# Kernel optimization log

Measured on AMD Instinct MI355X. Metric: run time of the kernel, lower is better.

## Reference

```python
import jax, jax.numpy as jnp
import numpy as np

DT = 0.1    # arg.DELTA_T
BOX = 1.0   # arg.WORLD_SIZE
B = 8388608


def range_angle(ang):
    # wrap angle to [-pi, pi)
    return jnp.mod(ang + np.pi, 2.0 * np.pi) - np.pi


def setup_inputs() -> dict:
    key = jax.random.key(0)
    k1, k2, k3, k4, k5, k6 = jax.random.split(key, 6)
    x = jax.random.normal(k1, (B, 5), dtype=jnp.float32)          # [px,py,ang,vel,ang_vel]
    a = jax.random.uniform(k2, (B, 2), dtype=jnp.float32)          # actions [a_v, a_w]
    noise = jax.random.normal(k3, (B, 2), dtype=jnp.float32)       # standard-normal process noise
    pro_gains = jax.random.uniform(k4, (2,), dtype=jnp.float32)    # process gains
    pro_noise_ln_vars = jax.random.normal(k5, (2,), dtype=jnp.float32)  # log-variances
    goal_radius = jax.random.uniform(k6, (1,), dtype=jnp.float32)
    return {"x": x, "a": a, "noise": noise, "pro_gains": pro_gains,
            "pro_noise_ln_vars": pro_noise_ln_vars, "goal_radius": goal_radius}


def reference(x, a, noise, pro_gains, pro_noise_ln_vars, goal_radius):
    px, py, ang = x[:, 0], x[:, 1], x[:, 2]
    # w = sqrt(exp(ln_var)) * randn(2)  (noise pre-sampled, deterministic)
    std = jnp.sqrt(jnp.exp(pro_noise_ln_vars))            # [2]
    w = std * noise                                        # [B,2]
    vel = pro_gains[0] * a[:, 0] + w[:, 0]                 # 0*vel drops old vel
    ang_vel = pro_gains[1] * a[:, 1] + w[:, 1]
    ang = range_angle(ang + ang_vel * DT)
    px = jnp.clip(px + vel * jnp.cos(ang) * DT, -BOX, BOX)
    py = jnp.clip(py + vel * jnp.sin(ang) * DT, -BOX, BOX)
    next_x = jnp.stack([px, py, ang, vel, ang_vel], axis=-1)   # [B,5]
    reached_target = jnp.sqrt(px * px + py * py) <= goal_radius[0]  # [B] bool
    return next_x, reached_target
```

## Files before the change

### kernel.cpp

```cpp
#include <hip/hip_runtime.h>
#include <math.h>


__global__ __launch_bounds__(256) void step_kernel(
    const float* __restrict__ x,
    const float* __restrict__ a,
    const float* __restrict__ noise,
    const float* __restrict__ pro_gains,
    const float* __restrict__ pro_noise_ln_vars,
    const float* __restrict__ goal_radius,
    float* __restrict__ out_next,
    float* __restrict__ out_reach,
    int n)
{
    int i = blockIdx.x * blockDim.x + threadIdx.x;
    if (i >= n) return;

    const float g0 = pro_gains[0];
    const float g1 = pro_gains[1];
    const float std0 = __fsqrt_rn(expf(pro_noise_ln_vars[0]));
    const float std1 = __fsqrt_rn(expf(pro_noise_ln_vars[1]));
    const float gr = goal_radius[0];

    const size_t si = (size_t)i;
    const float2 av = *(const float2*)(a + 2 * si);
    const float2 nv = *(const float2*)(noise + 2 * si);
    const float px0  = x[5 * si + 0];
    const float py0  = x[5 * si + 1];
    const float ang0 = x[5 * si + 2];

    const float w0 = __fmul_rn(std0, nv.x);
    const float w1 = __fmul_rn(std1, nv.y);
    const float vel     = __fadd_rn(__fmul_rn(g0, av.x), w0);
    const float ang_vel = __fadd_rn(__fmul_rn(g1, av.y), w1);

    const float DT     = 0.1f;
    const float PI_F   = 3.14159265358979323846f;
    const float TWOPI  = 6.283185307179586f;

    const float t  = __fadd_rn(ang0, __fmul_rn(ang_vel, DT));
    const float tp = __fadd_rn(t, PI_F);
    float m = fmodf(tp, TWOPI);
    if (m < 0.0f) m = __fadd_rn(m, TWOPI);
    const float ang = __fsub_rn(m, PI_F);

    float s, c;
    sincosf(ang, &s, &c);

    float px = __fadd_rn(px0, __fmul_rn(__fmul_rn(vel, c), DT));
    px = fminf(fmaxf(px, -1.0f), 1.0f);
    float py = __fadd_rn(py0, __fmul_rn(__fmul_rn(vel, s), DT));
    py = fminf(fmaxf(py, -1.0f), 1.0f);

    const float r2 = __fadd_rn(__fmul_rn(px, px), __fmul_rn(py, py));
    const float r  = __fsqrt_rn(r2);

    out_next[5 * si + 0] = px;
    out_next[5 * si + 1] = py;
    out_next[5 * si + 2] = ang;
    out_next[5 * si + 3] = vel;
    out_next[5 * si + 4] = ang_vel;
    out_reach[si] = (r <= gr) ? 1.0f : 0.0f;
}

extern "C" void kernel_launch(void* const* d_in, const int* in_sizes, int n_in,
                              void* d_out, int out_size, void* d_ws, size_t ws_size,
                              hipStream_t stream) {
    const float* x      = (const float*)d_in[0];
    const float* a      = (const float*)d_in[1];
    const float* noise  = (const float*)d_in[2];
    const float* gains  = (const float*)d_in[3];
    const float* lnvars = (const float*)d_in[4];
    const float* gradius= (const float*)d_in[5];

    const int n = in_sizes[0] / 5;
    float* out_next  = (float*)d_out;
    float* out_reach = (float*)d_out + (size_t)n * 5;

    const int block = 256;
    const int grid = (n + block - 1) / block;
    step_kernel<<<grid, block, 0, stream>>>(x, a, noise, gains, lnvars, gradius,
                                            out_next, out_reach, n);
}
```

Baseline: 395.3 us.

## Use grid-stride loop with software prefetch of next element's inputs

```diff
diff --git a/kernel.cpp b/kernel.cpp
--- a/kernel.cpp
+++ b/kernel.cpp
@@ -13,72 +13,98 @@
     float* __restrict__ out_reach,
     int n)
 {
+    const int stride = gridDim.x * blockDim.x;
     int i = blockIdx.x * blockDim.x + threadIdx.x;
     if (i >= n) return;
 
-    const float g0 = pro_gains[0];
-    const float g1 = pro_gains[1];
+    const float g0   = pro_gains[0];
+    const float g1   = pro_gains[1];
     const float std0 = __fsqrt_rn(expf(pro_noise_ln_vars[0]));
     const float std1 = __fsqrt_rn(expf(pro_noise_ln_vars[1]));
-    const float gr = goal_radius[0];
+    const float gr   = goal_radius[0];
 
-    const size_t si = (size_t)i;
-    const float2 av = *(const float2*)(a + 2 * si);
-    const float2 nv = *(const float2*)(noise + 2 * si);
-    const float px0  = x[5 * si + 0];
-    const float py0  = x[5 * si + 1];
-    const float ang0 = x[5 * si + 2];
+    const float DT    = 0.1f;
+    const float PI_F  = 3.14159265358979323846f;
+    const float TWOPI = 6.283185307179586f;
 
-    const float w0 = __fmul_rn(std0, nv.x);
-    const float w1 = __fmul_rn(std1, nv.y);
-    const float vel     = __fadd_rn(__fmul_rn(g0, av.x), w0);
-    const float ang_vel = __fadd_rn(__fmul_rn(g1, av.y), w1);
+    float2 av = *(const float2*)(a + 2 * (size_t)i);
+    float2 nv = *(const float2*)(noise + 2 * (size_t)i);
+    float px0  = x[5 * (size_t)i + 0];
+    float py0  = x[5 * (size_t)i + 1];
+    float ang0 = x[5 * (size_t)i + 2];
 
-    const float DT     = 0.1f;
-    const float PI_F   = 3.14159265358979323846f;
-    const float TWOPI  = 6.283185307179586f;
+    while (true) {
+        const int inext = i + stride;
+        const bool have_next = inext < n;
+        float2 av2, nv2;
+        float px2 = 0.f, py2 = 0.f, ang2 = 0.f;
+        av2.x = av2.y = nv2.x = nv2.y = 0.f;
+        if (have_next) {
+            const size_t sj = (size_t)inext;
+            av2  = *(const float2*)(a + 2 * sj);
+            nv2  = *(const float2*)(noise + 2 * sj);
+            px2  = x[5 * sj + 0];
+            py2  = x[5 * sj + 1];
+            ang2 = x[5 * sj + 2];
+        }
 
-    const float t  = __fadd_rn(ang0, __fmul_rn(ang_vel, DT));
-    const float tp = __fadd_rn(t, PI_F);
-    float m = fmodf(tp, TWOPI);
-    if (m < 0.0f) m = __fadd_rn(m, TWOPI);
-    const float ang = __fsub_rn(m, PI_F);
+        const float w0 = __fmul_rn(std0, nv.x);
+        const float w1 = __fmul_rn(std1, nv.y);
+        const float vel     = __fadd_rn(__fmul_rn(g0, av.x), w0);
+        const float ang_vel = __fadd_rn(__fmul_rn(g1, av.y), w1);
 
-    float s, c;
-    sincosf(ang, &s, &c);
+        const float t  = __fadd_rn(ang0, __fmul_rn(ang_vel, DT));
+        const float tp = __fadd_rn(t, PI_F);
+        float m = fmodf(tp, TWOPI);
+        if (m < 0.0f) m = __fadd_rn(m, TWOPI);
+        const float ang = __fsub_rn(m, PI_F);
 
-    float px = __fadd_rn(px0, __fmul_rn(__fmul_rn(vel, c), DT));
-    px = fminf(fmaxf(px, -1.0f), 1.0f);
-    float py = __fadd_rn(py0, __fmul_rn(__fmul_rn(vel, s), DT));
-    py = fminf(fmaxf(py, -1.0f), 1.0f);
+        float s, c;
+        sincosf(ang, &s, &c);
 
-    const float r2 = __fadd_rn(__fmul_rn(px, px), __fmul_rn(py, py));
-    const float r  = __fsqrt_rn(r2);
+        float px = __fadd_rn(px0, __fmul_rn(__fmul_rn(vel, c), DT));
+        px = fminf(fmaxf(px, -1.0f), 1.0f);
+        float py = __fadd_rn(py0, __fmul_rn(__fmul_rn(vel, s), DT));
+        py = fminf(fmaxf(py, -1.0f), 1.0f);
 
-    out_next[5 * si + 0] = px;
-    out_next[5 * si + 1] = py;
-    out_next[5 * si + 2] = ang;
-    out_next[5 * si + 3] = vel;
-    out_next[5 * si + 4] = ang_vel;
-    out_reach[si] = (r <= gr) ? 1.0f : 0.0f;
+        const float r2 = __fadd_rn(__fmul_rn(px, px), __fmul_rn(py, py));
+        const float r  = __fsqrt_rn(r2);
+        const float rch = (r <= gr) ? 1.0f : 0.0f;
+
+        const size_t si = (size_t)i;
+        out_next[5 * si + 0] = px;
+        out_next[5 * si + 1] = py;
+        out_next[5 * si + 2] = ang;
+        out_next[5 * si + 3] = vel;
+        out_next[5 * si + 4] = ang_vel;
+        out_reach[si] = rch;
+
+        if (!have_next) break;
+        i = inext;
+        av = av2; nv = nv2; px0 = px2; py0 = py2; ang0 = ang2;
+    }
 }
 
 extern "C" void kernel_launch(void* const* d_in, const int* in_sizes, int n_in,
                               void* d_out, int out_size, void* d_ws, size_t ws_size,
                               hipStream_t stream) {
-    const float* x      = (const float*)d_in[0];
-    const float* a      = (const float*)d_in[1];
-    const float* noise  = (const float*)d_in[2];
-    const float* gains  = (const float*)d_in[3];
-    const float* lnvars = (const float*)d_in[4];
-    const float* gradius= (const float*)d_in[5];
+    const float* x       = (const float*)d_in[0];
+    const float* a       = (const float*)d_in[1];
+    const float* noise   = (const float*)d_in[2];
+    const float* gains   = (const float*)d_in[3];
+    const float* lnvars  = (const float*)d_in[4];
+    const float* gradius = (const float*)d_in[5];
 
     const int n = in_sizes[0] / 5;
     float* out_next  = (float*)d_out;
     float* out_reach = (float*)d_out + (size_t)n * 5;
 
     const int block = 256;
-    const int grid = (n + block - 1) / block;
+    int grid = 2048;
+    const long long total_threads_needed = ((long long)n + 0);
+    if ((long long)grid * block > total_threads_needed)
+        grid = (int)((total_threads_needed + block - 1) / block);
+    if (grid < 1) grid = 1;
     step_kernel<<<grid, block, 0, stream>>>(x, a, noise, gains, lnvars, gradius,
                                             out_next, out_reach, n);
 }
```

Result: no change. 402.2 us (+1.7%).
